# Performance work log

Measured on AMD Instinct MI355X. Metric: run time of the kernel, lower is better.

Reference implementation:

```python
import jax, jax.numpy as jnp
import numpy as np

D = 768
H = 8
HD = D // H  # 96
DFF = 2048
EPS = 1e-5


def layernorm(x, g, b):
    mu = jnp.mean(x, axis=-1, keepdims=True)
    var = jnp.var(x, axis=-1, keepdims=True)
    return (x - mu) * jax.lax.rsqrt(var + EPS) * g + b


def setup_inputs() -> dict:
    key = jax.random.key(0)
    ks = jax.random.split(key, 12)
    B, L = 4, 1024
    s = lambda fan: 1.0 / np.sqrt(fan)
    return {
        "x": jax.random.normal(ks[0], (B, L, D), jnp.float32),
        "attn_bias": jax.random.normal(ks[1], (B, L, L), jnp.float32),
        "in_proj_w": jax.random.normal(ks[2], (3 * D, D), jnp.float32) * s(D),
        "in_proj_b": jnp.zeros((3 * D,), jnp.float32),
        "out_w": jax.random.normal(ks[3], (D, D), jnp.float32) * s(D),
        "out_b": jnp.zeros((D,), jnp.float32),
        "ff1_w": jax.random.normal(ks[4], (DFF, D), jnp.float32) * s(D),
        "ff1_b": jnp.zeros((DFF,), jnp.float32),
        "ff2_w": jax.random.normal(ks[5], (D, DFF), jnp.float32) * s(DFF),
        "ff2_b": jnp.zeros((D,), jnp.float32),
        "ln1_g": jnp.ones((D,), jnp.float32),
        "ln1_b": jnp.zeros((D,), jnp.float32),
        "ln2_g": jnp.ones((D,), jnp.float32),
        "ln2_b": jnp.zeros((D,), jnp.float32),
    }


def reference(x, attn_bias, in_proj_w, in_proj_b, out_w, out_b,
              ff1_w, ff1_b, ff2_w, ff2_b, ln1_g, ln1_b, ln2_g, ln2_b):
    B, L, _ = x.shape
    # combined QKV projection (torch nn.MultiheadAttention in_proj)
    qkv = x @ in_proj_w.T + in_proj_b  # [B,L,3D]
    q, k, v = jnp.split(qkv, 3, axis=-1)
    q = q.reshape(B, L, H, HD).transpose(0, 2, 1, 3)  # [B,H,L,hd]
    k = k.reshape(B, L, H, HD).transpose(0, 2, 1, 3)
    v = v.reshape(B, L, H, HD).transpose(0, 2, 1, 3)
    scale = 1.0 / np.sqrt(HD)
    scores = jnp.einsum('bhld,bhmd->bhlm', q, k) * scale + attn_bias[:, None, :, :]
    probs = jax.nn.softmax(scores, axis=-1)
    attn = jnp.einsum('bhlm,bhmd->bhld', probs, v)  # [B,H,L,hd]
    attn = attn.transpose(0, 2, 1, 3).reshape(B, L, D)
    attn = attn @ out_w.T + out_b
    x = layernorm(x + attn, ln1_g, ln1_b)
    h = jax.nn.gelu(x @ ff1_w.T + ff1_b, approximate=False) @ ff2_w.T + ff2_b
    x = layernorm(x + h, ln2_g, ln2_b)
    return x
```

## Files before the change

### kernel.cpp

```cpp
#include <hip/hip_runtime.h>

typedef __bf16 bf16x8 __attribute__((ext_vector_type(8)));
typedef float f32x4 __attribute__((ext_vector_type(4)));
typedef unsigned short u16x8 __attribute__((ext_vector_type(8)));
typedef short s16x4 __attribute__((ext_vector_type(4)));

__device__ __forceinline__ unsigned short f2b(float f) {
    union { float f; unsigned u; } v; v.f = f;
    unsigned r = (v.u + 0x7fffu + ((v.u >> 16) & 1u)) >> 16;
    return (unsigned short)r;
}

__device__ __forceinline__ void load_lds16(const void* g, void* l) {
    __builtin_amdgcn_global_load_lds(
        (const __attribute__((address_space(1))) unsigned int*)g,
        (__attribute__((address_space(3))) unsigned int*)l,
        16, 0, 0);
}

__global__ void cvt5_kernel(const float* __restrict__ s0, const float* __restrict__ s1,
                            const float* __restrict__ s2, const float* __restrict__ s3,
                            const float* __restrict__ s4,
                            unsigned short* __restrict__ d0, unsigned short* __restrict__ d1,
                            unsigned short* __restrict__ d2, unsigned short* __restrict__ d3,
                            unsigned short* __restrict__ d4) {
    int i = blockIdx.x * 256 + threadIdx.x;
    const float* s; unsigned short* d; int off;
    if (i < 786432)       { s = s0; d = d0; off = 0; }
    else if (i < 1228800) { s = s1; d = d1; off = 786432; }
    else if (i < 1376256) { s = s2; d = d2; off = 1228800; }
    else if (i < 1769472) { s = s3; d = d3; off = 1376256; }
    else                  { s = s4; d = d4; off = 1769472; }
    i -= off;
    f32x4 v = ((const f32x4*)s)[i];
    s16x4 o;
    o.x = (short)f2b(v.x);
    o.y = (short)f2b(v.y);
    o.z = (short)f2b(v.z);
    o.w = (short)f2b(v.w);
    ((s16x4*)d)[i] = o;
}

template <int EPI>
__global__ __launch_bounds__(256, 5)
void gemm_ho(const unsigned short* __restrict__ A, const unsigned short* __restrict__ Bm,
             const float* __restrict__ bias, void* __restrict__ Cout,
             int M, int N, int K) {
    __shared__ unsigned short As[2][64 * 64];
    __shared__ unsigned short Bs[2][64 * 64];
    const int tid = threadIdx.x, lane = tid & 63, wid = tid >> 6;
    const int l15 = lane & 15, lq = lane >> 4;
    const int wr = wid >> 1, wc = wid & 1;

    const int nwg = gridDim.x * gridDim.y;
    int bid = blockIdx.y * gridDim.x + blockIdx.x;
    bid = (bid & 7) * (nwg >> 3) + (bid >> 3);
    const int bx = bid % gridDim.x, by = bid / gridDim.x;
    const int m0 = by * 64, n0 = bx * 64;

    const int srow = lane >> 3;
    const int scol = ((lane & 7) ^ srow) * 8;
    const int sw = (l15 & 7) << 4;

    f32x4 acc[2][2];
#pragma unroll
    for (int i = 0; i < 2; i++)
#pragma unroll
        for (int j = 0; j < 2; j++) acc[i][j] = 0.0f;

    auto stage = [&](int buf, int kt) {
        const int kb = kt * 64;
#pragma unroll
        for (int i = 0; i < 4; ++i) {
            const int c = wid * 4 + i;
            if (c < 8) {
                load_lds16(A + (size_t)(m0 + c * 8 + srow) * K + kb + scol,
                           (char*)As[buf] + c * 1024);
            } else {
                load_lds16(Bm + (size_t)(n0 + (c - 8) * 8 + srow) * K + kb + scol,
                           (char*)Bs[buf] + (c - 8) * 1024);
            }
        }
    };

    auto compute = [&](int buf) {
#pragma unroll
        for (int kc = 0; kc < 2; ++kc) {
            const int cb = kc * 64;
            bf16x8 af[2], bf[2];
#pragma unroll
            for (int mi = 0; mi < 2; mi++) {
                const int row = wr * 32 + mi * 16 + l15;
                af[mi] = *(const bf16x8*)((const char*)As[buf] + row * 128 + ((cb + lq * 16) ^ sw));
            }
#pragma unroll
            for (int ni = 0; ni < 2; ni++) {
                const int row = wc * 32 + ni * 16 + l15;
                bf[ni] = *(const bf16x8*)((const char*)Bs[buf] + row * 128 + ((cb + lq * 16) ^ sw));
            }
#pragma unroll
            for (int mi = 0; mi < 2; mi++)
#pragma unroll
                for (int ni = 0; ni < 2; ni++)
                    acc[mi][ni] = __builtin_amdgcn_mfma_f32_16x16x32_bf16(af[mi], bf[ni], acc[mi][ni], 0, 0, 0);
        }
    };

    const int nkt = K / 64;
    stage(0, 0);
    stage(1, 1);
    asm volatile("s_waitcnt vmcnt(4)" ::: "memory");
    __builtin_amdgcn_s_barrier();
    int cur = 0;
    for (int t = 0; t < nkt; ++t) {
        compute(cur);
        __builtin_amdgcn_s_barrier();
        if (t + 2 < nkt) {
            stage(cur, t + 2);
            asm volatile("s_waitcnt vmcnt(4)" ::: "memory");
        } else if (t + 1 < nkt) {
            asm volatile("s_waitcnt vmcnt(0)" ::: "memory");
        }
        if (t + 1 < nkt) __builtin_amdgcn_s_barrier();
        cur ^= 1;
    }

#pragma unroll
    for (int mi = 0; mi < 2; mi++) {
#pragma unroll
        for (int ni = 0; ni < 2; ni++) {
            const int col = n0 + wc * 32 + ni * 16 + l15;
            const float bv = bias[col];
#pragma unroll
            for (int r = 0; r < 4; r++) {
                const int row = m0 + wr * 32 + mi * 16 + lq * 4 + r;
                float v = acc[mi][ni][r] + bv;
                if constexpr (EPI == 2) {
                    v = 0.5f * v * (1.0f + erff(v * 0.7071067811865475f));
                }
                if constexpr (EPI == 1) {
                    ((float*)Cout)[(size_t)row * N + col] = v;
                } else {
                    ((unsigned short*)Cout)[(size_t)row * N + col] = f2b(v);
                }
            }
        }
    }
}

__global__ __launch_bounds__(256, 2)
void attn_kernel(const unsigned short* __restrict__ qkv,
                 const float* __restrict__ bias,
                 unsigned short* __restrict__ out) {
    const int L = 1024, TD = 2304, HD = 96;
    const int qt = blockIdx.x, h = blockIdx.y, b = blockIdx.z;
    const int tid = threadIdx.x, lane = tid & 63, wid = tid >> 6;
    const int l15 = lane & 15, lq = lane >> 4;
    const int q0 = qt * 64;
    const float scale = 0.10206207261596576f;

    __shared__ unsigned short Ks[64][104];
    __shared__ unsigned short Vt[96][72];
    __shared__ unsigned short Ps[4][16][72];
    __shared__ float Ot[4][16][100];

    bf16x8 qf[3];
    const int qrow = q0 + wid * 16 + l15;
#pragma unroll
    for (int kc = 0; kc < 3; kc++)
        qf[kc] = *(const bf16x8*)(qkv + (size_t)(b * L + qrow) * TD + h * HD + kc * 32 + lq * 8);

    f32x4 o[6];
#pragma unroll
    for (int df = 0; df < 6; df++) o[df] = 0.0f;
    float mrow[4] = {-1e30f, -1e30f, -1e30f, -1e30f};
    float lrow[4] = {0.f, 0.f, 0.f, 0.f};

    for (int kv0 = 0; kv0 < L; kv0 += 64) {
#pragma unroll
        for (int i = 0; i < 3; i++) {
            int c = i * 256 + tid;
            int row = c / 12, cc = c % 12;
            *(f32x4*)&Ks[row][cc * 8] =
                *(const f32x4*)(qkv + (size_t)(b * L + kv0 + row) * TD + 768 + h * HD + cc * 8);
        }
#pragma unroll
        for (int i = 0; i < 3; i++) {
            int dblk = i * 4 + wid;
            int m = lane;
            u16x8 v = *(const u16x8*)(qkv + (size_t)(b * L + kv0 + m) * TD + 1536 + h * HD + dblk * 8);
#pragma unroll
            for (int j = 0; j < 8; j++) Vt[dblk * 8 + j][m] = v[j];
        }
        __syncthreads();

        f32x4 s[4];
#pragma unroll
        for (int nf = 0; nf < 4; nf++) s[nf] = 0.0f;
#pragma unroll
        for (int kc = 0; kc < 3; kc++) {
#pragma unroll
            for (int nf = 0; nf < 4; nf++) {
                bf16x8 kf = *(const bf16x8*)&Ks[nf * 16 + l15][kc * 32 + lq * 8];
                s[nf] = __builtin_amdgcn_mfma_f32_16x16x32_bf16(qf[kc], kf, s[nf], 0, 0, 0);
            }
        }
#pragma unroll
        for (int nf = 0; nf < 4; nf++) {
            int colg = kv0 + nf * 16 + l15;
#pragma unroll
            for (int r = 0; r < 4; r++) {
                int rowg = q0 + wid * 16 + lq * 4 + r;
                s[nf][r] = s[nf][r] * scale + bias[((size_t)b * L + rowg) * L + colg];
            }
        }
        float pm[4];
#pragma unroll
        for (int r = 0; r < 4; r++) {
            float mx = fmaxf(fmaxf(s[0][r], s[1][r]), fmaxf(s[2][r], s[3][r]));
#pragma unroll
            for (int d = 1; d < 16; d <<= 1) mx = fmaxf(mx, __shfl_xor(mx, d, 64));
            pm[r] = mx;
        }
        float alpha[4];
#pragma unroll
        for (int r = 0; r < 4; r++) {
            float mn = fmaxf(mrow[r], pm[r]);
            alpha[r] = __expf(mrow[r] - mn);
            mrow[r] = mn;
        }
        float rs[4] = {0.f, 0.f, 0.f, 0.f};
#pragma unroll
        for (int nf = 0; nf < 4; nf++)
#pragma unroll
            for (int r = 0; r < 4; r++) {
                float p = __expf(s[nf][r] - mrow[r]);
                s[nf][r] = p;
                rs[r] += p;
            }
#pragma unroll
        for (int r = 0; r < 4; r++) {
#pragma unroll
            for (int d = 1; d < 16; d <<= 1) rs[r] += __shfl_xor(rs[r], d, 64);
            lrow[r] = lrow[r] * alpha[r] + rs[r];
        }
#pragma unroll
        for (int nf = 0; nf < 4; nf++)
#pragma unroll
            for (int r = 0; r < 4; r++)
                Ps[wid][lq * 4 + r][nf * 16 + l15] = f2b(s[nf][r]);
#pragma unroll
        for (int df = 0; df < 6; df++)
#pragma unroll
            for (int r = 0; r < 4; r++) o[df][r] *= alpha[r];
        asm volatile("s_waitcnt lgkmcnt(0)" ::: "memory");
#pragma unroll
        for (int kc = 0; kc < 2; kc++) {
            bf16x8 pf = *(const bf16x8*)&Ps[wid][l15][kc * 32 + lq * 8];
#pragma unroll
            for (int df = 0; df < 6; df++) {
                bf16x8 vf = *(const bf16x8*)&Vt[df * 16 + l15][kc * 32 + lq * 8];
                o[df] = __builtin_amdgcn_mfma_f32_16x16x32_bf16(pf, vf, o[df], 0, 0, 0);
            }
        }
        __syncthreads();
    }

#pragma unroll
    for (int r = 0; r < 4; r++) {
        float inv = 1.0f / lrow[r];
        const int rl = lq * 4 + r;
#pragma unroll
        for (int df = 0; df < 6; df++) {
            const int cl = df * 16 + l15;
            Ot[wid][rl][cl ^ (lq << 3)] = o[df][r] * inv;
        }
    }
    asm volatile("s_waitcnt lgkmcnt(0)" ::: "memory");
    {
        const int r = lane >> 2, c8 = lane & 3;
        const int rowg = q0 + wid * 16 + r;
#pragma unroll
        for (int it = 0; it < 3; it++) {
            const int oc = c8 + 4 * it;
            const int po = oc ^ ((r >> 2) & 3);
            f32x4 a = *(const f32x4*)&Ot[wid][r][po * 8];
            f32x4 bb = *(const f32x4*)&Ot[wid][r][po * 8 + 4];
            u16x8 p;
#pragma unroll
            for (int e = 0; e < 4; e++) { p[e] = f2b(a[e]); p[e + 4] = f2b(bb[e]); }
            *(u16x8*)&out[((size_t)b * L + rowg) * 768 + h * 96 + oc * 8] = p;
        }
    }
}

template <int WRITE_B>
__global__ __launch_bounds__(256, 4)
void ln_kernel(const float* __restrict__ x, const float* __restrict__ res,
               const float* __restrict__ g, const float* __restrict__ bvec,
               float* __restrict__ outf, unsigned short* __restrict__ outb) {
    const int Dm = 768;
    int row = blockIdx.x;
    int tid = threadIdx.x;
    f32x4 v = {0.f, 0.f, 0.f, 0.f};
    float sum = 0.f, sq = 0.f;
    if (tid < 192) {
        f32x4 xv = ((const f32x4*)(x + (size_t)row * Dm))[tid];
        f32x4 rv = ((const f32x4*)(res + (size_t)row * Dm))[tid];
        v = xv + rv;
        sum = v.x + v.y + v.z + v.w;
        sq = v.x * v.x + v.y * v.y + v.z * v.z + v.w * v.w;
    }
#pragma unroll
    for (int d = 1; d < 64; d <<= 1) {
        sum += __shfl_xor(sum, d, 64);
        sq += __shfl_xor(sq, d, 64);
    }
    __shared__ float ps[8];
    int lane = tid & 63, wid = tid >> 6;
    if (lane == 0) { ps[wid] = sum; ps[wid + 4] = sq; }
    __syncthreads();
    sum = ps[0] + ps[1] + ps[2] + ps[3];
    sq = ps[4] + ps[5] + ps[6] + ps[7];
    float mu = sum * (1.0f / 768.0f);
    float var = sq * (1.0f / 768.0f) - mu * mu;
    float rsg = rsqrtf(var + 1e-5f);
    if (tid < 192) {
        f32x4 gv = ((const f32x4*)g)[tid];
        f32x4 bv = ((const f32x4*)bvec)[tid];
        f32x4 ov;
#pragma unroll
        for (int e = 0; e < 4; e++) ov[e] = (v[e] - mu) * rsg * gv[e] + bv[e];
        ((f32x4*)(outf + (size_t)row * Dm))[tid] = ov;
        if constexpr (WRITE_B) {
            s16x4 pb;
#pragma unroll
            for (int e = 0; e < 4; e++) pb[e] = (short)f2b(ov[e]);
            ((s16x4*)(outb + (size_t)row * Dm))[tid] = pb;
        }
    }
}

extern "C" void kernel_launch(void* const* d_in, const int* in_sizes, int n_in,
                              void* d_out, int out_size, void* d_ws, size_t ws_size,
                              hipStream_t stream) {
    (void)in_sizes; (void)n_in; (void)out_size; (void)ws_size;
    const float* x         = (const float*)d_in[0];
    const float* attn_bias = (const float*)d_in[1];
    const float* in_proj_w = (const float*)d_in[2];
    const float* in_proj_b = (const float*)d_in[3];
    const float* out_w     = (const float*)d_in[4];
    const float* out_b     = (const float*)d_in[5];
    const float* ff1_w     = (const float*)d_in[6];
    const float* ff1_b     = (const float*)d_in[7];
    const float* ff2_w     = (const float*)d_in[8];
    const float* ff2_b     = (const float*)d_in[9];
    const float* ln1_g     = (const float*)d_in[10];
    const float* ln1_b     = (const float*)d_in[11];
    const float* ln2_g     = (const float*)d_in[12];
    const float* ln2_b     = (const float*)d_in[13];

    const int NTOK = 4096;
    char* ws = (char*)d_ws;
    size_t off = 0;
    auto alloc = [&](size_t bytes) { void* p = ws + off; off += (bytes + 255) & ~(size_t)255; return p; };
    unsigned short* xb    = (unsigned short*)alloc((size_t)NTOK * 768 * 2);
    unsigned short* wqkv  = (unsigned short*)alloc((size_t)2304 * 768 * 2);
    unsigned short* wout  = (unsigned short*)alloc((size_t)768 * 768 * 2);
    unsigned short* wff1  = (unsigned short*)alloc((size_t)2048 * 768 * 2);
    unsigned short* wff2  = (unsigned short*)alloc((size_t)768 * 2048 * 2);
    unsigned short* qkvb  = (unsigned short*)alloc((size_t)NTOK * 2304 * 2);
    unsigned short* attnb = (unsigned short*)alloc((size_t)NTOK * 768 * 2);
    float*          aproj = (float*)alloc((size_t)NTOK * 768 * 4);
    float*          x1f   = (float*)alloc((size_t)NTOK * 768 * 4);
    unsigned short* x1b   = (unsigned short*)alloc((size_t)NTOK * 768 * 2);
    unsigned short* h1b  = qkvb;
    float*          ff2o = aproj;

    cvt5_kernel<<<dim3(8448), 256, 0, stream>>>(x, in_proj_w, out_w, ff1_w, ff2_w,
                                                xb, wqkv, wout, wff1, wff2);

    gemm_ho<0><<<dim3(2304 / 64, NTOK / 64), 256, 0, stream>>>(xb, wqkv, in_proj_b, qkvb, NTOK, 2304, 768);
    attn_kernel<<<dim3(16, 8, 4), 256, 0, stream>>>(qkvb, attn_bias, attnb);
    gemm_ho<1><<<dim3(768 / 64, NTOK / 64), 256, 0, stream>>>(attnb, wout, out_b, aproj, NTOK, 768, 768);
    ln_kernel<1><<<dim3(NTOK), 256, 0, stream>>>(x, aproj, ln1_g, ln1_b, x1f, x1b);
    gemm_ho<2><<<dim3(2048 / 64, NTOK / 64), 256, 0, stream>>>(x1b, wff1, ff1_b, h1b, NTOK, 2048, 768);
    gemm_ho<1><<<dim3(768 / 64, NTOK / 64), 256, 0, stream>>>(h1b, wff2, ff2_b, ff2o, NTOK, 768, 2048);
    ln_kernel<0><<<dim3(NTOK), 256, 0, stream>>>(x1f, ff2o, ln2_g, ln2_b, (float*)d_out, nullptr);
}
```

Before: 168.6 us.

## Split attention over KV halves with separate merge kernel

```diff
diff --git a/kernel.cpp b/kernel.cpp
--- a/kernel.cpp
+++ b/kernel.cpp
@@ -148,21 +148,25 @@
     }
 }
 
-__global__ __launch_bounds__(256, 2)
-void attn_kernel(const unsigned short* __restrict__ qkv,
-                 const float* __restrict__ bias,
-                 unsigned short* __restrict__ out) {
-    const int L = 1024, TD = 2304, HD = 96;
-    const int qt = blockIdx.x, h = blockIdx.y, b = blockIdx.z;
+__global__ __launch_bounds__(256, 4)
+void attn_split(const unsigned short* __restrict__ qkv,
+                const float* __restrict__ bias,
+                float* __restrict__ O0, float* __restrict__ O1,
+                float2* __restrict__ ml) {
+    const int L = 1024, TD = 2304, HD = 96, NTOK = 4096;
+    const int qt = blockIdx.x, h = blockIdx.y;
+    const int b = blockIdx.z >> 1, half = blockIdx.z & 1;
+    float* __restrict__ Op = half ? O1 : O0;
     const int tid = threadIdx.x, lane = tid & 63, wid = tid >> 6;
     const int l15 = lane & 15, lq = lane >> 4;
     const int q0 = qt * 64;
     const float scale = 0.10206207261596576f;
 
-    __shared__ unsigned short Ks[64][104];
-    __shared__ unsigned short Vt[96][72];
-    __shared__ unsigned short Ps[4][16][72];
-    __shared__ float Ot[4][16][100];
+    __shared__ char smem[36352];
+    unsigned short (*Ks)[104]    = (unsigned short (*)[104])smem;
+    unsigned short (*Vt)[72]     = (unsigned short (*)[72])(smem + 13312);
+    unsigned short (*Ps)[16][72] = (unsigned short (*)[16][72])(smem + 27136);
+    float (*Ot)[16][100]         = (float (*)[16][100])smem;
 
     bf16x8 qf[3];
     const int qrow = q0 + wid * 16 + l15;
@@ -176,7 +180,8 @@
     float mrow[4] = {-1e30f, -1e30f, -1e30f, -1e30f};
     float lrow[4] = {0.f, 0.f, 0.f, 0.f};
 
-    for (int kv0 = 0; kv0 < L; kv0 += 64) {
+    const int kvbeg = half * 512, kvend = kvbeg + 512;
+    for (int kv0 = kvbeg; kv0 < kvend; kv0 += 64) {
 #pragma unroll
         for (int i = 0; i < 3; i++) {
             int c = i * 256 + tid;
@@ -266,14 +271,21 @@
         __syncthreads();
     }
 
+    if (l15 == 0) {
+#pragma unroll
+        for (int r = 0; r < 4; r++) {
+            const int rowg = q0 + wid * 16 + lq * 4 + r;
+            float2 v; v.x = mrow[r]; v.y = lrow[r];
+            ml[((size_t)half * NTOK + (size_t)b * L + rowg) * 8 + h] = v;
+        }
+    }
 #pragma unroll
     for (int r = 0; r < 4; r++) {
-        float inv = 1.0f / lrow[r];
         const int rl = lq * 4 + r;
 #pragma unroll
         for (int df = 0; df < 6; df++) {
             const int cl = df * 16 + l15;
-            Ot[wid][rl][cl ^ (lq << 3)] = o[df][r] * inv;
+            Ot[wid][rl][cl ^ (lq << 3)] = o[df][r];
         }
     }
     asm volatile("s_waitcnt lgkmcnt(0)" ::: "memory");
@@ -286,12 +298,29 @@
             const int po = oc ^ ((r >> 2) & 3);
             f32x4 a = *(const f32x4*)&Ot[wid][r][po * 8];
             f32x4 bb = *(const f32x4*)&Ot[wid][r][po * 8 + 4];
-            u16x8 p;
-#pragma unroll
-            for (int e = 0; e < 4; e++) { p[e] = f2b(a[e]); p[e + 4] = f2b(bb[e]); }
-            *(u16x8*)&out[((size_t)b * L + rowg) * 768 + h * 96 + oc * 8] = p;
-        }
-    }
+            *(f32x4*)&Op[((size_t)b * L + rowg) * 768 + h * 96 + oc * 8] = a;
+            *(f32x4*)&Op[((size_t)b * L + rowg) * 768 + h * 96 + oc * 8 + 4] = bb;
+        }
+    }
+}
+
+__global__ __launch_bounds__(192, 8)
+void attn_merge(const float* __restrict__ O0, const float* __restrict__ O1,
+                const float2* __restrict__ ml, unsigned short* __restrict__ out) {
+    const int NTOK = 4096;
+    const int row = blockIdx.x, tid = threadIdx.x;
+    const int h = tid / 24;
+    float2 a = ml[(size_t)row * 8 + h];
+    float2 b = ml[((size_t)NTOK + row) * 8 + h];
+    float m = fmaxf(a.x, b.x);
+    float e0 = __expf(a.x - m), e1 = __expf(b.x - m);
+    float linv = 1.0f / (a.y * e0 + b.y * e1);
+    f32x4 v0 = ((const f32x4*)(O0 + (size_t)row * 768))[tid];
+    f32x4 v1 = ((const f32x4*)(O1 + (size_t)row * 768))[tid];
+    s16x4 p;
+#pragma unroll
+    for (int e = 0; e < 4; e++) p[e] = (short)f2b((v0[e] * e0 + v1[e] * e1) * linv);
+    ((s16x4*)(out + (size_t)row * 768))[tid] = p;
 }
 
 template <int WRITE_B>
@@ -376,12 +405,16 @@
     unsigned short* x1b   = (unsigned short*)alloc((size_t)NTOK * 768 * 2);
     unsigned short* h1b  = qkvb;
     float*          ff2o = aproj;
+    float*          O0   = aproj;
+    float*          O1   = x1f;
+    float2*         mlb  = (float2*)x1b;
 
     cvt5_kernel<<<dim3(8448), 256, 0, stream>>>(x, in_proj_w, out_w, ff1_w, ff2_w,
                                                 xb, wqkv, wout, wff1, wff2);
 
     gemm_ho<0><<<dim3(2304 / 64, NTOK / 64), 256, 0, stream>>>(xb, wqkv, in_proj_b, qkvb, NTOK, 2304, 768);
-    attn_kernel<<<dim3(16, 8, 4), 256, 0, stream>>>(qkvb, attn_bias, attnb);
+    attn_split<<<dim3(16, 8, 8), 256, 0, stream>>>(qkvb, attn_bias, O0, O1, mlb);
+    attn_merge<<<dim3(NTOK), 192, 0, stream>>>(O0, O1, mlb, attnb);
     gemm_ho<1><<<dim3(768 / 64, NTOK / 64), 256, 0, stream>>>(attnb, wout, out_b, aproj, NTOK, 768, 768);
     ln_kernel<1><<<dim3(NTOK), 256, 0, stream>>>(x, aproj, ln1_g, ln1_b, x1f, x1b);
     gemm_ho<2><<<dim3(2048 / 64, NTOK / 64), 256, 0, stream>>>(x1b, wff1, ff1_b, h1b, NTOK, 2048, 768);
```

After: 174.4 us. 3.5% more time.
